# Kernel optimization log

Hardware: AMD Instinct MI355X
Metric: run time of the kernel (lower is better)

## Reference

```python
import jax, jax.numpy as jnp
import numpy as np

NUM_CLASSES = 80
D_IMG = 2048
D_WORD = 300
D_MID = 1024
B = 8
CONV = 14


def setup_inputs() -> dict:
    key = jax.random.key(0)
    ks = jax.random.split(key, 6)
    s = lambda k, shape, sc: jax.random.normal(k, shape, dtype=jnp.float32) * sc
    return {
        "batch_size": B,
        "img_feature_map": jax.random.normal(ks[0], (B, D_IMG, CONV, CONV), dtype=jnp.float32),
        "word_features": jax.random.normal(ks[1], (NUM_CLASSES, D_WORD), dtype=jnp.float32),
        "W1": s(ks[2], (D_MID, D_IMG), 0.02),
        "W2": s(ks[3], (D_MID, D_WORD), 0.02),
        "W3": s(ks[4], (D_MID, D_MID), 0.02),
        "b3": jnp.zeros((D_MID,), jnp.float32),
        "Wa": s(ks[5], (1, D_MID), 0.02),
        "ba": jnp.zeros((1,), jnp.float32),
    }


def reference(batch_size, img_feature_map, word_features, W1, W2, W3, b3, Wa, ba):
    # img_feature_map: [B, D_img, H, W] -> [B, H, W, D_img] (matches torch double transpose)
    Bn, D, H, W = img_feature_map.shape
    fmap = jnp.transpose(img_feature_map, (0, 2, 3, 1))                 # [B,H,W,D]
    f_wh = jnp.einsum('bhwd,md->bhwm', fmap, W1)                        # fc_1: [B,H,W,M]
    f_wd = word_features @ W2.T                                         # fc_2: [C,M]
    # broadcast multiply (no explicit repeat) + tanh
    t = jnp.tanh(f_wh[:, :, :, None, :] * f_wd)                         # [B,H,W,C,M]
    lb = jnp.einsum('bhwcm,nm->bhwcn', t, W3) + b3                      # fc_3: [B,H,W,C,M]
    coef = jnp.einsum('bhwcm,m->bhwc', lb, Wa[0]) + ba[0]               # fc_a: [B,H,W,C]
    # softmax over spatial positions per (batch, class)
    C = coef.shape[-1]
    coef = jax.nn.softmax(coef.reshape(Bn, H * W, C), axis=1).reshape(Bn, H, W, C)
    # softmax-weighted spatial pooling -> [B, C, D]
    return jnp.einsum('bhwc,bhwd->bcd', coef, fmap)
```

## Files before the change

kernel.cpp:

```cpp
#include <hip/hip_runtime.h>
#include <hip/hip_bf16.h>
#include <stdint.h>

#define NB 8
#define DIMG 2048
#define HWN 196
#define PN 1568
#define DMID 1024
#define NC 80
#define DWORD 300
#define PART 4

typedef short bf16x8 __attribute__((ext_vector_type(8)));
typedef float f32x4 __attribute__((ext_vector_type(4)));
typedef float f32x2 __attribute__((ext_vector_type(2)));

__device__ __forceinline__ unsigned short f2bf(float x) {
  union { float f; unsigned u; } c; c.f = x;
  unsigned r = c.u + 0x7FFFu + ((c.u >> 16) & 1u);
  return (unsigned short)(r >> 16);
}

__global__ void k_tc(const float* __restrict__ img, float* __restrict__ fmap,
                     unsigned short* __restrict__ fmapH,
                     const float* __restrict__ W1, unsigned short* __restrict__ W1h) {
  __shared__ float tile[64][33];
  int bx = blockIdx.x;
  int tx = threadIdx.x, ty = threadIdx.y;
  if (bx < 1792) {
    int d0 = (bx & 31) * 64;
    int rem = bx >> 5;
    int h0 = (rem % 7) * 32, b = rem / 7;
    const float* src = img + (size_t)b * DIMG * HWN;
#pragma unroll
    for (int i = 0; i < 64; i += 8) {
      int hw = h0 + tx;
      tile[ty + i][tx] = (hw < HWN) ? src[(size_t)(d0 + ty + i) * HWN + hw] : 0.f;
    }
    __syncthreads();
#pragma unroll
    for (int i = 0; i < 32; i += 8) {
      int hw = h0 + ty + i;
      if (hw < HWN) {
        int d = tx * 2;
        float v0 = tile[d][ty + i], v1 = tile[d + 1][ty + i];
        size_t o = (size_t)(b * HWN + hw) * DIMG + d0 + d;
        f32x2 fv = {v0, v1};
        *(f32x2*)&fmap[o] = fv;
        unsigned hv = (unsigned)f2bf(v0) | ((unsigned)f2bf(v1) << 16);
        *(unsigned*)&fmapH[o] = hv;
      }
    }
  } else {
    int tid = ty * 32 + tx;
    int i = ((bx - 1792) * 256 + tid) * 4;
    f32x4 v = *(const f32x4*)(W1 + i);
    ushort4 s;
    s.x = f2bf(v[0]); s.y = f2bf(v[1]); s.z = f2bf(v[2]); s.w = f2bf(v[3]);
    *(ushort4*)(W1h + i) = s;
  }
}

#define GLDS(g, l) \
  __builtin_amdgcn_global_load_lds((const __attribute__((address_space(1))) void*)(g), \
                                   (__attribute__((address_space(3))) void*)(l), 16, 0, 0)

__global__ __launch_bounds__(256) void k_gw(const unsigned short* __restrict__ A,
                                            const unsigned short* __restrict__ Bw,
                                            float* __restrict__ C,
                                            const float* __restrict__ word,
                                            const float* __restrict__ W2,
                                            float* __restrict__ fwd,
                                            const float* __restrict__ Wa,
                                            const float* __restrict__ W3,
                                            float* __restrict__ partial) {
  __shared__ __align__(16) char smem[38400];
  int bz = blockIdx.x;
  int t = threadIdx.x;
  if (bz < 208) {
    unsigned short* As = (unsigned short*)smem;
    unsigned short* Bs = As + 4096;
    int m0 = (bz % 13) * 128;
    int n0 = ((bz / 13) & 7) * 128;
    int koff = (bz / 104) * 1024;
    int w = t >> 6, l = t & 63;
    int wr = w >> 1, wc = w & 1;
    f32x4 zero = {0.f, 0.f, 0.f, 0.f};
    f32x4 acc[4][4];
#pragma unroll
    for (int i = 0; i < 4; ++i)
#pragma unroll
      for (int j = 0; j < 4; ++j) acc[i][j] = zero;

    int sr = t >> 2, sk = (t & 3) << 3;
    const unsigned short* ga0 = A + (size_t)(m0 + sr) * 2048 + koff + sk;
    const unsigned short* ga1 = A + (size_t)(m0 + 64 + sr) * 2048 + koff + sk;
    const unsigned short* gb0 = Bw + (size_t)(n0 + sr) * 2048 + koff + sk;
    const unsigned short* gb1 = Bw + (size_t)(n0 + 64 + sr) * 2048 + koff + sk;

    int fr = l & 15, ko = (l >> 4) << 3;

    for (int kk = 0; kk < 1024; kk += 32) {
      __syncthreads();
      GLDS(ga0 + kk, As + t * 8);
      GLDS(ga1 + kk, As + t * 8 + 2048);
      GLDS(gb0 + kk, Bs + t * 8);
      GLDS(gb1 + kk, Bs + t * 8 + 2048);
      __syncthreads();
      bf16x8 a[4], b[4];
#pragma unroll
      for (int i = 0; i < 4; ++i)
        a[i] = *(const bf16x8*)&As[(wr * 64 + i * 16 + fr) * 32 + ko];
#pragma unroll
      for (int j = 0; j < 4; ++j)
        b[j] = *(const bf16x8*)&Bs[(wc * 64 + j * 16 + fr) * 32 + ko];
#pragma unroll
      for (int i = 0; i < 4; ++i)
#pragma unroll
        for (int j = 0; j < 4; ++j)
          acc[i][j] = __builtin_amdgcn_mfma_f32_16x16x32_bf16(a[i], b[j], acc[i][j], 0, 0, 0);
    }
    float* Cz = C + (size_t)(bz / 104) * (1600 * DMID);
    int cr = (l >> 4) << 2, cc2 = l & 15;
#pragma unroll
    for (int i = 0; i < 4; ++i) {
#pragma unroll
      for (int q = 0; q < 4; ++q) {
        int row = m0 + wr * 64 + i * 16 + cr + q;
        if (row < 1600) {
#pragma unroll
          for (int j = 0; j < 4; ++j)
            Cz[(size_t)row * DMID + n0 + wc * 64 + j * 16 + cc2] = acc[i][j][q];
        }
      }
    }
  } else if (bz < 528) {
    float* w2s = (float*)smem;
    float* wds = w2s + 16 * 300;
    int idx = bz - 208;
    int m0 = (idx & 63) * 16, c0 = (idx >> 6) * 16;
    const float SC = 2.8853900817779268f;
    for (int u = t; u < 16 * 75; u += 256) {
      int r = u / 75, q = u - r * 75;
      *(f32x4*)&w2s[r * 300 + q * 4] = *(const f32x4*)(W2 + (size_t)(m0 + r) * DWORD + q * 4);
      f32x4 v = *(const f32x4*)(word + (size_t)(c0 + r) * DWORD + q * 4);
      *(f32x4*)&wds[r * 300 + q * 4] = v * SC;
    }
    __syncthreads();
    int ci = t >> 4, mi = t & 15;
    f32x4 av = {0.f, 0.f, 0.f, 0.f};
    const float* wr_ = &wds[ci * 300];
    const float* w2r = &w2s[mi * 300];
    for (int q = 0; q < 75; ++q) {
      f32x4 wv = *(const f32x4*)&wr_[q * 4];
      f32x4 bv = *(const f32x4*)&w2r[q * 4];
#pragma unroll
      for (int u = 0; u < 4; ++u) av[u] = fmaf(wv[u], bv[u], av[u]);
    }
    fwd[(size_t)(c0 + ci) * DMID + m0 + mi] = av[0] + av[1] + av[2] + av[3];
  } else {
    int idx = bz - 528;
    int m = (idx & 3) * 256 + t;
    int n0 = (idx >> 2) * 64;
    float acc = 0.f;
#pragma unroll 4
    for (int n = n0; n < n0 + 64; ++n) acc = fmaf(Wa[n], W3[(size_t)n * DMID + m], acc);
    partial[(size_t)(idx >> 2) * DMID + m] = acc;
  }
}

#define MC 64
__global__ __launch_bounds__(256) void k_coef(const float* __restrict__ fwhp,
                                              const float* __restrict__ fwd,
                                              const float* __restrict__ partial,
                                              float* __restrict__ coefp) {
  __shared__ __align__(16) float al[32][68];
  __shared__ __align__(16) float bl[16][68];
  __shared__ __align__(16) float wl[MC];
  int p0 = blockIdx.x * 32, c0 = blockIdx.y * 16, mz = blockIdx.z;
  int t = threadIdx.x;
  int pi = t >> 4, ci = t & 15;
  float acc[2] = {0.f, 0.f};
  const size_t FS = (size_t)1600 * DMID;

  for (int mc = 0; mc < 4; ++mc) {
    int mbase = mz * 256 + mc * MC;
    __syncthreads();
    {
      int sra = t >> 3, sca = (t & 7) << 3;
      const float* gA = fwhp + (size_t)(p0 + sra) * DMID + mbase + sca;
#pragma unroll
      for (int q = 0; q < 2; ++q) {
        f32x4 v = *(const f32x4*)&gA[q * 4];
        v += *(const f32x4*)&gA[FS + q * 4];
        *(f32x4*)&al[sra][sca + q * 4] = v;
      }
      int srb = t >> 4, scb = (t & 15) << 2;
      *(f32x4*)&bl[srb][scb] = *(const f32x4*)(fwd + (size_t)(c0 + srb) * DMID + mbase + scb);
      if (t < MC) {
        float v = 0.f;
#pragma unroll
        for (int s = 0; s < 16; ++s) v += partial[(size_t)s * DMID + mbase + t];
        wl[t] = -2.f * v;
      }
    }
    __syncthreads();
    for (int mm = 0; mm < MC; mm += 4) {
      f32x4 wv = *(const f32x4*)&wl[mm];
      f32x4 bv = *(const f32x4*)&bl[ci][mm];
      f32x4 av0 = *(const f32x4*)&al[pi][mm];
      f32x4 av1 = *(const f32x4*)&al[pi + 16][mm];
#pragma unroll
      for (int u = 0; u < 4; ++u) {
        float w = wv[u], b = bv[u];
        float e0 = __builtin_amdgcn_exp2f(av0[u] * b);
        float e1 = __builtin_amdgcn_exp2f(av1[u] * b);
        acc[0] = fmaf(w, __builtin_amdgcn_rcpf(1.f + e0), acc[0]);
        acc[1] = fmaf(w, __builtin_amdgcn_rcpf(1.f + e1), acc[1]);
      }
    }
  }
  float* cp = coefp + (size_t)mz * (PN * NC);
#pragma unroll
  for (int j = 0; j < 2; ++j) {
    int p = p0 + pi + 16 * j;
    if (p < PN) cp[(size_t)p * NC + c0 + ci] = acc[j];
  }
}

__global__ __launch_bounds__(256) void k_pool(const float* __restrict__ coefp,
                                              const float* __restrict__ fmap,
                                              float* __restrict__ out) {
  __shared__ __align__(16) float wt[HWN][16];
  __shared__ float red[16][16];
  __shared__ float mxs[16], inv[16];
  int dc = blockIdx.x * 256, cg = blockIdx.y * 16, b = blockIdx.z;
  int t = threadIdx.x;
  for (int i = t; i < HWN * 4; i += 256) {
    int hw = i >> 2, j4 = (i & 3) << 2;
    size_t o = (size_t)(b * HWN + hw) * NC + cg + j4;
    f32x4 s = {0.f, 0.f, 0.f, 0.f};
#pragma unroll
    for (int z = 0; z < PART; ++z) s += *(const f32x4*)&coefp[o + (size_t)z * (PN * NC)];
    *(f32x4*)&wt[hw][j4] = s;
  }
  __syncthreads();
  int j = t & 15, g = t >> 4;
  float pm = -1e30f;
  for (int hw = g; hw < HWN; hw += 16) pm = fmaxf(pm, wt[hw][j]);
  red[g][j] = pm;
  __syncthreads();
  if (t < 16) {
    float m = red[0][t];
#pragma unroll
    for (int g2 = 1; g2 < 16; ++g2) m = fmaxf(m, red[g2][t]);
    mxs[t] = m;
  }
  __syncthreads();
  float mj = mxs[j], ps = 0.f;
  for (int hw = g; hw < HWN; hw += 16) {
    float e = __builtin_amdgcn_exp2f((wt[hw][j] - mj) * 1.4426950408889634f);
    wt[hw][j] = e;
    ps += e;
  }
  red[g][j] = ps;
  __syncthreads();
  if (t < 16) {
    float s = 0.f;
#pragma unroll
    for (int g2 = 0; g2 < 16; ++g2) s += red[g2][t];
    inv[t] = 1.f / s;
  }
  __syncthreads();
  float acc[16];
#pragma unroll
  for (int q = 0; q < 16; ++q) acc[q] = 0.f;
  const float* fp = fmap + (size_t)b * HWN * DIMG + dc + t;
  for (int h4 = 0; h4 < HWN / 4; ++h4) {
    float v0 = fp[(size_t)(h4 * 4 + 0) * DIMG];
    float v1 = fp[(size_t)(h4 * 4 + 1) * DIMG];
    float v2 = fp[(size_t)(h4 * 4 + 2) * DIMG];
    float v3 = fp[(size_t)(h4 * 4 + 3) * DIMG];
#pragma unroll
    for (int q = 0; q < 16; ++q) {
      acc[q] = fmaf(wt[h4 * 4 + 0][q], v0, acc[q]);
      acc[q] = fmaf(wt[h4 * 4 + 1][q], v1, acc[q]);
      acc[q] = fmaf(wt[h4 * 4 + 2][q], v2, acc[q]);
      acc[q] = fmaf(wt[h4 * 4 + 3][q], v3, acc[q]);
    }
  }
#pragma unroll
  for (int q = 0; q < 16; ++q)
    out[((size_t)b * NC + cg + q) * DIMG + dc + t] = acc[q] * inv[q];
}

extern "C" void kernel_launch(void* const* d_in, const int* in_sizes, int n_in,
                              void* d_out, int out_size, void* d_ws, size_t ws_size,
                              hipStream_t stream) {
  const float* img  = (const float*)d_in[1];
  const float* word = (const float*)d_in[2];
  const float* W1   = (const float*)d_in[3];
  const float* W2   = (const float*)d_in[4];
  const float* W3   = (const float*)d_in[5];
  const float* Wa   = (const float*)d_in[7];
  float* out = (float*)d_out;
  char* ws = (char*)d_ws;

  float*          fmap    = (float*)(ws + 0);
  unsigned short* fmapH   = (unsigned short*)(ws + 12845056);
  unsigned short* W1h     = (unsigned short*)(ws + 19660800);
  float*          fwhp    = (float*)(ws + 23855104);
  float*          fwd     = (float*)(ws + 36962304);
  float*          partial = (float*)(ws + 37355520);
  float*          coefp   = (float*)(ws + 37421056);

  hipLaunchKernelGGL(k_tc, dim3(3840), dim3(32, 8), 0, stream, img, fmap, fmapH, W1, W1h);
  hipLaunchKernelGGL(k_gw, dim3(592), dim3(256), 0, stream,
                     fmapH, W1h, fwhp, word, W2, fwd, Wa, W3, partial);
  hipLaunchKernelGGL(k_coef, dim3(49, 5, 4), dim3(256), 0, stream, fwhp, fwd, partial, coefp);
  hipLaunchKernelGGL(k_pool, dim3(8, 5, 8), dim3(256), 0, stream, coefp, fmap, out);
  (void)in_sizes; (void)n_in; (void)out_size; (void)ws_size;
}
```

Measured before the change: 99.50 us.

## Triple-buffer GEMM LDS tiles with async loads and XOR swizzle

Converts the fc_1 bf16 GEMM main loop from a single LDS buffer with two barriers per K step into a three-stage ring, so global-to-LDS loads for tile k+2 are issued while tile k is computed, with one barrier per step gated by vmcnt. It also XOR-swizzles the 16-byte column chunks in LDS to reduce bank conflicts on the fragment reads. Shared memory grows from 38400 to 49152 bytes, which may lower occupancy for every block of this fused kernel. The manual waitcnt and sched_barrier make correctness depend on exact counts of outstanding loads.

```diff
diff --git a/kernel.cpp b/kernel.cpp
--- a/kernel.cpp
+++ b/kernel.cpp
@@ -74,12 +74,12 @@
                                             const float* __restrict__ Wa,
                                             const float* __restrict__ W3,
                                             float* __restrict__ partial) {
-  __shared__ __align__(16) char smem[38400];
+  __shared__ __align__(16) char smem[49152];
   int bz = blockIdx.x;
   int t = threadIdx.x;
   if (bz < 208) {
     unsigned short* As = (unsigned short*)smem;
-    unsigned short* Bs = As + 4096;
+    unsigned short* Bs = As + 3 * 4096;
     int m0 = (bz % 13) * 128;
     int n0 = ((bz / 13) & 7) * 128;
     int koff = (bz / 104) * 1024;
@@ -92,33 +92,57 @@
 #pragma unroll
       for (int j = 0; j < 4; ++j) acc[i][j] = zero;
 
-    int sr = t >> 2, sk = (t & 3) << 3;
-    const unsigned short* ga0 = A + (size_t)(m0 + sr) * 2048 + koff + sk;
-    const unsigned short* ga1 = A + (size_t)(m0 + 64 + sr) * 2048 + koff + sk;
-    const unsigned short* gb0 = Bw + (size_t)(n0 + sr) * 2048 + koff + sk;
-    const unsigned short* gb1 = Bw + (size_t)(n0 + 64 + sr) * 2048 + koff + sk;
-
-    int fr = l & 15, ko = (l >> 4) << 3;
-
-    for (int kk = 0; kk < 1024; kk += 32) {
-      __syncthreads();
-      GLDS(ga0 + kk, As + t * 8);
-      GLDS(ga1 + kk, As + t * 8 + 2048);
-      GLDS(gb0 + kk, Bs + t * 8);
-      GLDS(gb1 + kk, Bs + t * 8 + 2048);
-      __syncthreads();
-      bf16x8 a[4], b[4];
-#pragma unroll
-      for (int i = 0; i < 4; ++i)
-        a[i] = *(const bf16x8*)&As[(wr * 64 + i * 16 + fr) * 32 + ko];
-#pragma unroll
-      for (int j = 0; j < 4; ++j)
-        b[j] = *(const bf16x8*)&Bs[(wc * 64 + j * 16 + fr) * 32 + ko];
-#pragma unroll
-      for (int i = 0; i < 4; ++i)
-#pragma unroll
-        for (int j = 0; j < 4; ++j)
-          acc[i][j] = __builtin_amdgcn_mfma_f32_16x16x32_bf16(a[i], b[j], acc[i][j], 0, 0, 0);
+    int r0 = t >> 2, c0 = t & 3;
+    int swz = (c0 ^ (r0 & 3)) << 3;
+    const unsigned short* ga0 = A + (size_t)(m0 + r0) * 2048 + koff + swz;
+    const unsigned short* ga1 = A + (size_t)(m0 + 64 + r0) * 2048 + koff + swz;
+    const unsigned short* gb0 = Bw + (size_t)(n0 + r0) * 2048 + koff + swz;
+    const unsigned short* gb1 = Bw + (size_t)(n0 + 64 + r0) * 2048 + koff + swz;
+
+    int fr = l & 15, cc = l >> 4;
+    int aswz = (cc ^ (fr & 3)) << 3;
+    int a_base = (wr * 64 + fr) * 32 + aswz;
+    int b_base = (wc * 64 + fr) * 32 + aswz;
+
+#define STAGE(bi, kk) do { \
+    GLDS(ga0 + (kk), As + (bi) * 4096 + t * 8); \
+    GLDS(ga1 + (kk), As + (bi) * 4096 + t * 8 + 2048); \
+    GLDS(gb0 + (kk), Bs + (bi) * 4096 + t * 8); \
+    GLDS(gb1 + (kk), Bs + (bi) * 4096 + t * 8 + 2048); \
+  } while (0)
+#define COMPUTE(bi) do { \
+    const unsigned short* ap = As + (bi) * 4096; \
+    const unsigned short* bp = Bs + (bi) * 4096; \
+    bf16x8 a[4], b[4]; \
+    _Pragma("unroll") \
+    for (int i = 0; i < 4; ++i) a[i] = *(const bf16x8*)&ap[a_base + i * 512]; \
+    _Pragma("unroll") \
+    for (int j = 0; j < 4; ++j) b[j] = *(const bf16x8*)&bp[b_base + j * 512]; \
+    _Pragma("unroll") \
+    for (int i = 0; i < 4; ++i) \
+      _Pragma("unroll") \
+      for (int j = 0; j < 4; ++j) \
+        acc[i][j] = __builtin_amdgcn_mfma_f32_16x16x32_bf16(a[i], b[j], acc[i][j], 0, 0, 0); \
+  } while (0)
+
+    STAGE(0, 0);
+    STAGE(1, 32);
+    asm volatile("s_waitcnt vmcnt(4)" ::: "memory");
+    __builtin_amdgcn_s_barrier();
+    __builtin_amdgcn_sched_barrier(0);
+    for (int kt = 0; kt < 32; ++kt) {
+      int cur = kt % 3;
+      if (kt < 30) STAGE((kt + 2) % 3, (kt + 2) * 32);
+      COMPUTE(cur);
+      if (kt < 30) {
+        asm volatile("s_waitcnt vmcnt(4)" ::: "memory");
+        __builtin_amdgcn_s_barrier();
+        __builtin_amdgcn_sched_barrier(0);
+      } else if (kt == 30) {
+        asm volatile("s_waitcnt vmcnt(0)" ::: "memory");
+        __builtin_amdgcn_s_barrier();
+        __builtin_amdgcn_sched_barrier(0);
+      }
     }
     float* Cz = C + (size_t)(bz / 104) * (1600 * DMID);
     int cr = (l >> 4) << 2, cc2 = l & 15;
@@ -134,6 +158,8 @@
         }
       }
     }
+#undef STAGE
+#undef COMPUTE
   } else if (bz < 528) {
     float* w2s = (float*)smem;
     float* wds = w2s + 16 * 300;
```

Measured after the change: 92.09 us, median of 2. 7.4% less time.
